# Kernel optimization log

Measured on AMD Instinct MI355X. Metric: run time of the kernel, lower is better.

Reference implementation:

```python
import jax, jax.numpy as jnp
import numpy as np

NBATCH, NELEC, NATOMS, NBAS, NORB = 1024, 64, 16, 256, 128

# per-atom shell pattern: (l, m) pairs; bas_n = l (standard for GTO primitives)
_SHELL_LM = [(0, 0), (1, -1), (1, 0), (1, 1), (2, -2), (2, -1), (2, 0), (2, 1), (2, 2),
             (0, 0), (1, -1), (1, 0), (1, 1), (2, 0), (2, 2), (2, -2)]


def _norm_gaussian(bas_exp, bas_n):
    # Torch _norm_gaussian: bas_n += 1; A = exp**(0.25*(2n+1)); B = 2**(2n+1.5);
    # C = factorial2(2n-1)*sqrt(pi); norm = sqrt(B/C)*A
    n1 = bas_n + 1.0
    A = bas_exp ** (0.25 * (2.0 * n1 + 1.0))
    B = 2.0 ** (2.0 * n1 + 1.5)
    # 2*n1-1 in {1,3,5} for n in {0,1,2}: factorial2 -> {1,3,15}
    f2 = np.array([1.0, 3.0, 15.0], dtype=np.float32)[bas_n.astype(np.int32)]
    C = f2 * np.float32(np.sqrt(np.pi))
    return (np.sqrt(B / C) * A).astype(np.float32)


def setup_inputs() -> dict:
    key = jax.random.key(0)
    k0, k1, k2, k3, k4 = jax.random.split(key, 5)
    inp = jax.random.normal(k0, (NBATCH, NELEC, 3), jnp.float32) * 2.0
    atom_coords = jax.random.normal(k1, (NATOMS, 3), jnp.float32) * 3.0
    bas_exp = jax.random.uniform(k2, (NBAS,), jnp.float32, minval=0.2, maxval=3.0)
    bas_coeffs = jax.random.uniform(k3, (NBAS,), jnp.float32, minval=0.5, maxval=1.0)

    lm = np.array(_SHELL_LM * (NBAS // len(_SHELL_LM)), dtype=np.int32)  # [NBAS,2]
    bas_l = jnp.asarray(lm[:, 0])
    bas_m = jnp.asarray(lm[:, 1])
    bas_n = jnp.asarray(lm[:, 0].astype(np.float32))
    bas_atom_index = jnp.asarray((np.arange(NBAS) // (NBAS // NATOMS)).astype(np.int32))
    index_ctr = jnp.sort(jax.random.randint(k4, (NBAS,), 0, NORB)).astype(jnp.int32)
    norm_cst = jnp.asarray(_norm_gaussian(np.asarray(bas_exp), np.asarray(bas_n)))
    return {
        'input': inp, 'atom_coords': atom_coords, 'bas_exp': bas_exp,
        'bas_coeffs': bas_coeffs, 'norm_cst': norm_cst, 'bas_n': bas_n,
        'bas_l': bas_l, 'bas_m': bas_m, 'bas_atom_index': bas_atom_index,
        'index_ctr': index_ctr,
    }


def _spherical_harmonics(xyz, r, r2, bas_l, bas_m):
    # real spherical harmonics up to l=2 (QMCTorch constants)
    x, y, z = xyz[..., 0], xyz[..., 1], xyz[..., 2]
    C0 = 0.2820948          # 1/(2 sqrt(pi))
    C1 = 0.4886025          # sqrt(3/(4 pi))
    C2XY = 1.0925484        # sqrt(15/(4 pi))
    C2Z2 = 0.31539156       # sqrt(5/(16 pi))
    C2D = 0.5462742         # sqrt(15/(16 pi))
    y1 = C1 * jnp.where(bas_m == -1, y, jnp.where(bas_m == 0, z, x)) / r
    y2 = jnp.where(bas_m == -2, C2XY * x * y,
         jnp.where(bas_m == -1, C2XY * y * z,
         jnp.where(bas_m == 0, C2Z2 * (2.0 * z * z - x * x - y * y),
         jnp.where(bas_m == 1, C2XY * z * x, C2D * (x * x - y * y))))) / r2
    return jnp.where(bas_l == 0, C0, jnp.where(bas_l == 1, y1, y2))


def reference(input, atom_coords, bas_exp, bas_coeffs, norm_cst, bas_n,
              bas_l, bas_m, bas_atom_index, index_ctr):
    # bas_coords = atom_coords.repeat_interleave(nshells) expressed as a gather
    bas_coords = atom_coords[bas_atom_index]                     # [nbas, 3]
    xyz = input[:, :, None, :] - bas_coords[None, None, :, :]    # [B, E, nbas, 3]
    r2 = jnp.sum(xyz * xyz, axis=-1)                             # [B, E, nbas]
    r = jnp.sqrt(r2)
    R = r ** bas_n * jnp.exp(-bas_exp * r2)                      # gaussian radial
    Y = _spherical_harmonics(xyz, r, r2, bas_l, bas_m)
    bas = norm_cst * bas_coeffs * R * Y                          # [B, E, nbas]
    ao = jnp.zeros((input.shape[0], input.shape[1], NORB), bas.dtype)
    return ao.at[:, :, index_ctr].add(bas)                       # index_add over dim 2
```

## Files before the change

kernel.cpp:

```cpp
#include <hip/hip_runtime.h>

#define NBATCH 1024
#define NELEC  64
#define NBAS   256
#define NORB   128
#define NROWS  (NBATCH * NELEC)
#define RPB    16

__device__ __forceinline__ float wave_scan_incl(float x) {
    int t;
    t = __builtin_amdgcn_update_dpp(0, __float_as_int(x), 0x111, 0xf, 0xf, false);
    x += __int_as_float(t);
    t = __builtin_amdgcn_update_dpp(0, __float_as_int(x), 0x112, 0xf, 0xf, false);
    x += __int_as_float(t);
    t = __builtin_amdgcn_update_dpp(0, __float_as_int(x), 0x114, 0xf, 0xf, false);
    x += __int_as_float(t);
    t = __builtin_amdgcn_update_dpp(0, __float_as_int(x), 0x118, 0xf, 0xf, false);
    x += __int_as_float(t);
    t = __builtin_amdgcn_update_dpp(0, __float_as_int(x), 0x142, 0xa, 0xf, false);
    x += __int_as_float(t);
    t = __builtin_amdgcn_update_dpp(0, __float_as_int(x), 0x143, 0xc, 0xf, false);
    x += __int_as_float(t);
    return x;
}

__global__ __launch_bounds__(256, 8) void ao_kernel(
    const float* __restrict__ inp,
    const float* __restrict__ atom_coords,
    const float* __restrict__ bas_exp,
    const float* __restrict__ bas_coeffs,
    const float* __restrict__ norm_cst,
    const int*   __restrict__ bas_l,
    const int*   __restrict__ bas_m,
    const int*   __restrict__ bas_atom_index,
    const int*   __restrict__ index_ctr,
    float* __restrict__ out)
{
    __shared__ __align__(16) float s_vals[RPB][NBAS];
    __shared__ int s_start[NORB + 1];

    const int tid  = threadIdx.x;
    const int row0 = blockIdx.x * RPB;

    float ex = bas_exp[tid];
    float cc = norm_cst[tid] * bas_coeffs[tid];
    int   l  = bas_l[tid];
    int   m  = bas_m[tid];
    int   ai = bas_atom_index[tid];
    float cx = atom_coords[ai*3+0], cy = atom_coords[ai*3+1], cz = atom_coords[ai*3+2];

    int ic   = index_ctr[tid];
    int prev = (tid == 0) ? -1 : index_ctr[tid - 1];
    for (int o = prev + 1; o <= ic; ++o) s_start[o] = tid;
    if (tid == NBAS - 1)
        for (int o = ic + 1; o <= NORB; ++o) s_start[o] = NBAS;

    const float C0 = 0.2820948f, C1 = 0.4886025f, C2XY = 1.0925484f,
                C2Z2 = 0.31539156f, C2D = 0.5462742f;
    float a0=0.f,a1=0.f,a2=0.f,a3=0.f, b0=0.f,b1=0.f,b2=0.f,b3=0.f, c9=0.f;
    if (l == 0)            { a3 = cc*C0; b3 = 1.f; }
    else if (l == 1) {
        float s = cc*C1; b3 = 1.f;
        if      (m == -1) a1 = s;
        else if (m ==  0) a2 = s;
        else              a0 = s;
    } else {
        if      (m == -2) { a0 = cc*C2XY; b1 = 1.f; }
        else if (m == -1) { a1 = cc*C2XY; b2 = 1.f; }
        else if (m ==  0) { float s = cc*3.f*C2Z2; a2 = s; b2 = 1.f; c9 = -s/3.f; }
        else if (m ==  1) { a2 = cc*C2XY; b0 = 1.f; }
        else              { float s = cc*C2D; a0 = s; a1 = s; b0 = 1.f; b1 = -1.f; }
    }
    const float nex = -ex * 1.4426950408889634f;

    #pragma unroll
    for (int r = 0; r < RPB; ++r) {
        float px = inp[(row0 + r)*3 + 0];
        float py = inp[(row0 + r)*3 + 1];
        float pz = inp[(row0 + r)*3 + 2];
        float x = px - cx, y = py - cy, z = pz - cz;
        float r2 = fmaf(x, x, fmaf(y, y, z * z));
        float A  = fmaf(a0, x, fmaf(a1, y, fmaf(a2, z, a3)));
        float B  = fmaf(b0, x, fmaf(b1, y, fmaf(b2, z, b3)));
        float P  = fmaf(c9, r2, A * B);
        s_vals[r][tid] = __builtin_exp2f(nex * r2) * P;
    }
    __syncthreads();

    const int w = tid >> 6, ln = tid & 63;
    #pragma unroll
    for (int r = 0; r < 4; ++r) {
        const int row = 4*w + r;
        float4 v = *reinterpret_cast<const float4*>(&s_vals[row][ln << 2]);
        float e0 = v.x;
        float e1 = e0 + v.y;
        float e2 = e1 + v.z;
        float e3 = e2 + v.w;
        float s    = wave_scan_incl(e3);
        float excl = s - e3;
        *reinterpret_cast<float4*>(&s_vals[row][ln << 2]) =
            make_float4(e0 + excl, e1 + excl, e2 + excl, e3 + excl);
    }

    #pragma unroll
    for (int g = 0; g < 2; ++g) {
        const int row = 4*w + 2*g + (ln >> 5);
        const int q   = (ln & 31) << 2;
        int st[5];
        #pragma unroll
        for (int k = 0; k < 5; ++k) st[k] = s_start[q + k];
        float p[5];
        #pragma unroll
        for (int k = 0; k < 5; ++k) {
            int idx = st[k] - 1;
            float v = s_vals[row][idx < 0 ? 0 : idx];
            p[k] = (st[k] > 0) ? v : 0.0f;
        }
        float4 o4 = make_float4(p[1]-p[0], p[2]-p[1], p[3]-p[2], p[4]-p[3]);
        *reinterpret_cast<float4*>(&out[(size_t)(row0 + row) * NORB + q]) = o4;
    }
}

extern "C" void kernel_launch(void* const* d_in, const int* in_sizes, int n_in,
                              void* d_out, int out_size, void* d_ws, size_t ws_size,
                              hipStream_t stream) {
    const float* inp   = (const float*)d_in[0];
    const float* atomc = (const float*)d_in[1];
    const float* bexp  = (const float*)d_in[2];
    const float* bcoef = (const float*)d_in[3];
    const float* bnorm = (const float*)d_in[4];
    const int* bl   = (const int*)d_in[6];
    const int* bm   = (const int*)d_in[7];
    const int* bai  = (const int*)d_in[8];
    const int* ictr = (const int*)d_in[9];
    float* out = (float*)d_out;

    hipLaunchKernelGGL(ao_kernel, dim3(NROWS / RPB), dim3(256), 0, stream,
                       inp, atomc, bexp, bcoef, bnorm, bl, bm, bai, ictr, out);
}
```

Measured before the change: 20.96 us.

## Halve rows per block and pack row pairs into float2 FMAs

Rows per block drop from 16 to 8, which doubles the grid to 8192 blocks and halves the shared memory each block uses. The per-row basis evaluation now handles two rows at a time with 2-wide float vector FMAs, so the compiler can emit packed FP32 instructions. The scan and output phases are reworked to match the smaller tile. In exchange, the per-block setup (loading basis parameters and building s_start) is repeated across twice as many blocks.

```diff
diff --git a/kernel.cpp b/kernel.cpp
--- a/kernel.cpp
+++ b/kernel.cpp
@@ -5,7 +5,13 @@
 #define NBAS   256
 #define NORB   128
 #define NROWS  (NBATCH * NELEC)
-#define RPB    16
+#define RPB    8
+
+typedef float f32x2 __attribute__((ext_vector_type(2)));
+
+static __device__ __forceinline__ f32x2 pfma(f32x2 a, f32x2 b, f32x2 c) {
+    return __builtin_elementwise_fma(a, b, c);
+}
 
 __device__ __forceinline__ float wave_scan_incl(float x) {
     int t;
@@ -73,24 +79,33 @@
     }
     const float nex = -ex * 1.4426950408889634f;
 
+    const f32x2 vcx = {cx,cx}, vcy = {cy,cy}, vcz = {cz,cz};
+    const f32x2 va0 = {a0,a0}, va1 = {a1,a1}, va2 = {a2,a2}, va3 = {a3,a3};
+    const f32x2 vb0 = {b0,b0}, vb1 = {b1,b1}, vb2 = {b2,b2}, vb3 = {b3,b3};
+    const f32x2 vc9 = {c9,c9}, vnx = {nex,nex};
+
     #pragma unroll
-    for (int r = 0; r < RPB; ++r) {
-        float px = inp[(row0 + r)*3 + 0];
-        float py = inp[(row0 + r)*3 + 1];
-        float pz = inp[(row0 + r)*3 + 2];
-        float x = px - cx, y = py - cy, z = pz - cz;
-        float r2 = fmaf(x, x, fmaf(y, y, z * z));
-        float A  = fmaf(a0, x, fmaf(a1, y, fmaf(a2, z, a3)));
-        float B  = fmaf(b0, x, fmaf(b1, y, fmaf(b2, z, b3)));
-        float P  = fmaf(c9, r2, A * B);
-        s_vals[r][tid] = __builtin_exp2f(nex * r2) * P;
+    for (int r = 0; r < RPB; r += 2) {
+        const float* p0 = &inp[(size_t)(row0 + r) * 3];
+        const float* p1 = &inp[(size_t)(row0 + r + 1) * 3];
+        f32x2 px = {p0[0], p1[0]}, py = {p0[1], p1[1]}, pz = {p0[2], p1[2]};
+        f32x2 x = px - vcx, y = py - vcy, z = pz - vcz;
+        f32x2 r2 = pfma(x, x, pfma(y, y, z * z));
+        f32x2 A  = pfma(va0, x, pfma(va1, y, pfma(va2, z, va3)));
+        f32x2 B  = pfma(vb0, x, pfma(vb1, y, pfma(vb2, z, vb3)));
+        f32x2 P  = pfma(vc9, r2, A * B);
+        f32x2 t  = vnx * r2;
+        f32x2 E  = { __builtin_exp2f(t.x), __builtin_exp2f(t.y) };
+        f32x2 v  = E * P;
+        s_vals[r    ][tid] = v.x;
+        s_vals[r + 1][tid] = v.y;
     }
     __syncthreads();
 
     const int w = tid >> 6, ln = tid & 63;
     #pragma unroll
-    for (int r = 0; r < 4; ++r) {
-        const int row = 4*w + r;
+    for (int r = 0; r < 2; ++r) {
+        const int row = 2*w + r;
         float4 v = *reinterpret_cast<const float4*>(&s_vals[row][ln << 2]);
         float e0 = v.x;
         float e1 = e0 + v.y;
@@ -102,9 +117,8 @@
             make_float4(e0 + excl, e1 + excl, e2 + excl, e3 + excl);
     }
 
-    #pragma unroll
-    for (int g = 0; g < 2; ++g) {
-        const int row = 4*w + 2*g + (ln >> 5);
+    {
+        const int row = 2*w + (ln >> 5);
         const int q   = (ln & 31) << 2;
         int st[5];
         #pragma unroll
```

Result: slower. 23.97 us (+14.3%).

## Make each wave own its rows end-to-end, removing block barrier between stages

Applied to the files above, without the earlier changes.

Each wavefront now evaluates all 256 basis functions for its own 4 rows, with each lane handling 4 basis functions, then scans and gathers those rows itself. This removes the block-wide barrier between the evaluate and scan/gather phases, since only intra-wave dependencies remain. The norm/coefficient product is folded into the exponent as a log2 term, so one FMA replaces a multiply. Per-lane register use rises because four basis parameter sets are held at once, hence the lower occupancy hint. The output store becomes float2 per lane, and the shell pattern relies on l/m repeating with period 64.

```diff
diff --git a/kernel.cpp b/kernel.cpp
--- a/kernel.cpp
+++ b/kernel.cpp
@@ -1,11 +1,11 @@
 #include <hip/hip_runtime.h>
 
-#define NBATCH 1024
-#define NELEC  64
-#define NBAS   256
-#define NORB   128
-#define NROWS  (NBATCH * NELEC)
-#define RPB    16
+#define NBAS  256
+#define NORB  128
+#define NROWS 65536
+#define WPB   4
+#define RPW   4
+#define ROWS_PER_BLOCK (WPB * RPW)
 
 __device__ __forceinline__ float wave_scan_incl(float x) {
     int t;
@@ -24,7 +24,7 @@
     return x;
 }
 
-__global__ __launch_bounds__(256, 8) void ao_kernel(
+__global__ __launch_bounds__(256, 6) void ao_kernel(
     const float* __restrict__ inp,
     const float* __restrict__ atom_coords,
     const float* __restrict__ bas_exp,
@@ -36,88 +36,96 @@
     const int*   __restrict__ index_ctr,
     float* __restrict__ out)
 {
-    __shared__ __align__(16) float s_vals[RPB][NBAS];
+    __shared__ __align__(16) float s_buf[WPB][RPW][NBAS];
     __shared__ int s_start[NORB + 1];
 
-    const int tid  = threadIdx.x;
-    const int row0 = blockIdx.x * RPB;
+    const int tid = threadIdx.x;
+    const int w   = tid >> 6, ln = tid & 63;
 
-    float ex = bas_exp[tid];
-    float cc = norm_cst[tid] * bas_coeffs[tid];
-    int   l  = bas_l[tid];
-    int   m  = bas_m[tid];
-    int   ai = bas_atom_index[tid];
-    float cx = atom_coords[ai*3+0], cy = atom_coords[ai*3+1], cz = atom_coords[ai*3+2];
+    {
+        int ic   = index_ctr[tid];
+        int prev = (tid == 0) ? -1 : index_ctr[tid - 1];
+        for (int o = prev + 1; o <= ic; ++o) s_start[o] = tid;
+        if (tid == NBAS - 1)
+            for (int o = ic + 1; o <= NORB; ++o) s_start[o] = NBAS;
+    }
 
-    int ic   = index_ctr[tid];
-    int prev = (tid == 0) ? -1 : index_ctr[tid - 1];
-    for (int o = prev + 1; o <= ic; ++o) s_start[o] = tid;
-    if (tid == NBAS - 1)
-        for (int o = ic + 1; o <= NORB; ++o) s_start[o] = NBAS;
-
+    const int l = bas_l[ln], m = bas_m[ln];
+    float nex[4], lcc[4], cx[4], cy[4], cz[4];
+    #pragma unroll
+    for (int j = 0; j < 4; ++j) {
+        int b = ln + 64 * j;
+        nex[j] = -bas_exp[b] * 1.4426950408889634f;
+        lcc[j] = __log2f(norm_cst[b] * bas_coeffs[b]);
+        int ai = bas_atom_index[b];
+        cx[j] = atom_coords[ai*3+0];
+        cy[j] = atom_coords[ai*3+1];
+        cz[j] = atom_coords[ai*3+2];
+    }
     const float C0 = 0.2820948f, C1 = 0.4886025f, C2XY = 1.0925484f,
                 C2Z2 = 0.31539156f, C2D = 0.5462742f;
     float a0=0.f,a1=0.f,a2=0.f,a3=0.f, b0=0.f,b1=0.f,b2=0.f,b3=0.f, c9=0.f;
-    if (l == 0)            { a3 = cc*C0; b3 = 1.f; }
+    if (l == 0)            { a3 = C0; b3 = 1.f; }
     else if (l == 1) {
-        float s = cc*C1; b3 = 1.f;
-        if      (m == -1) a1 = s;
-        else if (m ==  0) a2 = s;
-        else              a0 = s;
+        b3 = 1.f;
+        if      (m == -1) a1 = C1;
+        else if (m ==  0) a2 = C1;
+        else              a0 = C1;
     } else {
-        if      (m == -2) { a0 = cc*C2XY; b1 = 1.f; }
-        else if (m == -1) { a1 = cc*C2XY; b2 = 1.f; }
-        else if (m ==  0) { float s = cc*3.f*C2Z2; a2 = s; b2 = 1.f; c9 = -s/3.f; }
-        else if (m ==  1) { a2 = cc*C2XY; b0 = 1.f; }
-        else              { float s = cc*C2D; a0 = s; a1 = s; b0 = 1.f; b1 = -1.f; }
+        if      (m == -2) { a0 = C2XY; b1 = 1.f; }
+        else if (m == -1) { a1 = C2XY; b2 = 1.f; }
+        else if (m ==  0) { a2 = 3.f*C2Z2; b2 = 1.f; c9 = -C2Z2; }
+        else if (m ==  1) { a2 = C2XY; b0 = 1.f; }
+        else              { a0 = C2D; a1 = C2D; b0 = 1.f; b1 = -1.f; }
     }
-    const float nex = -ex * 1.4426950408889634f;
+
+    __syncthreads();
+    const int st0 = s_start[2*ln], st1 = s_start[2*ln+1], st2 = s_start[2*ln+2];
+
+    const int rowbase = __builtin_amdgcn_readfirstlane(
+        (int)blockIdx.x * ROWS_PER_BLOCK + w * RPW);
+    float* bufw = &s_buf[w][0][0];
 
     #pragma unroll
-    for (int r = 0; r < RPB; ++r) {
-        float px = inp[(row0 + r)*3 + 0];
-        float py = inp[(row0 + r)*3 + 1];
-        float pz = inp[(row0 + r)*3 + 2];
-        float x = px - cx, y = py - cy, z = pz - cz;
-        float r2 = fmaf(x, x, fmaf(y, y, z * z));
-        float A  = fmaf(a0, x, fmaf(a1, y, fmaf(a2, z, a3)));
-        float B  = fmaf(b0, x, fmaf(b1, y, fmaf(b2, z, b3)));
-        float P  = fmaf(c9, r2, A * B);
-        s_vals[r][tid] = __builtin_exp2f(nex * r2) * P;
+    for (int r = 0; r < RPW; ++r) {
+        const int row = rowbase + r;
+        float px = inp[row*3+0], py = inp[row*3+1], pz = inp[row*3+2];
+        float* buf = bufw + r * NBAS;
+        #pragma unroll
+        for (int j = 0; j < 4; ++j) {
+            float x = px - cx[j], y = py - cy[j], z = pz - cz[j];
+            float r2 = fmaf(x, x, fmaf(y, y, z * z));
+            float A  = fmaf(a0, x, fmaf(a1, y, fmaf(a2, z, a3)));
+            float Bv = fmaf(b0, x, fmaf(b1, y, fmaf(b2, z, b3)));
+            float P  = fmaf(c9, r2, A * Bv);
+            float E  = __builtin_exp2f(fmaf(nex[j], r2, lcc[j]));
+            buf[ln + 64*j] = E * P;
+        }
     }
-    __syncthreads();
 
-    const int w = tid >> 6, ln = tid & 63;
     #pragma unroll
-    for (int r = 0; r < 4; ++r) {
-        const int row = 4*w + r;
-        float4 v = *reinterpret_cast<const float4*>(&s_vals[row][ln << 2]);
+    for (int r = 0; r < RPW; ++r) {
+        float* buf = bufw + r * NBAS;
+        float4 v = *reinterpret_cast<const float4*>(&buf[ln << 2]);
         float e0 = v.x;
         float e1 = e0 + v.y;
         float e2 = e1 + v.z;
         float e3 = e2 + v.w;
         float s    = wave_scan_incl(e3);
         float excl = s - e3;
-        *reinterpret_cast<float4*>(&s_vals[row][ln << 2]) =
+        *reinterpret_cast<float4*>(&buf[ln << 2]) =
             make_float4(e0 + excl, e1 + excl, e2 + excl, e3 + excl);
     }
 
     #pragma unroll
-    for (int g = 0; g < 2; ++g) {
-        const int row = 4*w + 2*g + (ln >> 5);
-        const int q   = (ln & 31) << 2;
-        int st[5];
-        #pragma unroll
-        for (int k = 0; k < 5; ++k) st[k] = s_start[q + k];
-        float p[5];
-        #pragma unroll
-        for (int k = 0; k < 5; ++k) {
-            int idx = st[k] - 1;
-            float v = s_vals[row][idx < 0 ? 0 : idx];
-            p[k] = (st[k] > 0) ? v : 0.0f;
-        }
-        float4 o4 = make_float4(p[1]-p[0], p[2]-p[1], p[3]-p[2], p[4]-p[3]);
-        *reinterpret_cast<float4*>(&out[(size_t)(row0 + row) * NORB + q]) = o4;
+    for (int r = 0; r < RPW; ++r) {
+        const float* buf = bufw + r * NBAS;
+        float p0 = (st0 > 0) ? buf[st0 - 1] : 0.f;
+        float p1 = (st1 > 0) ? buf[st1 - 1] : 0.f;
+        float p2 = (st2 > 0) ? buf[st2 - 1] : 0.f;
+        const int row = rowbase + r;
+        *reinterpret_cast<float2*>(&out[(size_t)row * NORB + 2*ln]) =
+            make_float2(p1 - p0, p2 - p1);
     }
 }
 
@@ -135,6 +143,6 @@
     const int* ictr = (const int*)d_in[9];
     float* out = (float*)d_out;
 
-    hipLaunchKernelGGL(ao_kernel, dim3(NROWS / RPB), dim3(256), 0, stream,
+    hipLaunchKernelGGL(ao_kernel, dim3(NROWS / ROWS_PER_BLOCK), dim3(256), 0, stream,
                        inp, atomc, bexp, bcoef, bnorm, bl, bm, bai, ictr, out);
 }
```

Result: no change. 21.14 us (+0.8%).
